# Optimization experiments

Hardware: AMD Instinct MI355X
Metric: run time of the kernel (lower is better)

## Reference

```python
import jax, jax.numpy as jnp
import numpy as np

NUM_EMBEDDINGS = 1024
EMBEDDING_DIM = 512
B, H, W = 32, 32, 32


def setup_inputs() -> dict:
    key = jax.random.key(0)
    k1, k2 = jax.random.split(key)
    z = jax.random.normal(k1, (B, EMBEDDING_DIM, H, W), dtype=jnp.float32)
    embedding = jax.random.normal(k2, (NUM_EMBEDDINGS, EMBEDDING_DIM), dtype=jnp.float32)
    return {"z": z, "embedding": embedding}


def reference(z, embedding):
    # z: [B, C, H, W] -> [B, H, W, C] -> [N, C]
    zp = jnp.transpose(z, (0, 2, 3, 1))
    b, h, w, d = zp.shape
    z_flat = zp.reshape(-1, d)
    # squared L2 distances: ||z||^2 - 2 z e^T + ||e||^2  -> [N, K]
    distances = (
        jnp.sum(z_flat ** 2, axis=1, keepdims=True)
        - 2.0 * (z_flat @ embedding.T)
        + jnp.sum(embedding ** 2, axis=1)
    )
    indices = jnp.argmin(distances, axis=1)  # [N]
    # one-hot @ embedding == direct gather
    quantized = embedding[indices]  # [N, d]
    quantized = quantized.reshape(b, h, w, d).transpose(0, 3, 1, 2)  # [B, C, H, W]
    return quantized, 0.0, indices.reshape(b, -1)
```

## Files before the change

### kernel.cpp

```cpp
#include <hip/hip_runtime.h>
#include <cfloat>

typedef _Float16 half8 __attribute__((ext_vector_type(8)));
typedef float    f32x4 __attribute__((ext_vector_type(4)));
typedef unsigned int  uint;
typedef unsigned short ushort;

constexpr int DIM  = 512;
constexpr int NEMB = 1024;
constexpr int HW   = 1024;
constexpr int NROW = 32 * HW;

constexpr long long QCOUNT = (long long)32 * 512 * 32 * 32;
constexpr long long SOFF   = QCOUNT;
constexpr long long IOFF   = SOFF + 1;

constexpr size_t WS_ZT    = 0;
constexpr size_t WS_ET    = 33554432;
constexpr size_t WS_ENORM = 34603008;
constexpr size_t WS_CNT   = 34607104;
constexpr size_t WS_LIST  = 34607360;
constexpr size_t WS_CANDB = WS_LIST + (size_t)NROW * 4;
constexpr size_t WS_CANDI = WS_CANDB + (size_t)2 * NROW * 8;
constexpr size_t WS_NEED  = WS_CANDI + (size_t)2 * NROW * 4;

constexpr float DELTA = 0.25f;

__device__ __forceinline__ void gld16(const void* g, void* l) {
    __builtin_amdgcn_global_load_lds(
        (const __attribute__((address_space(1))) void*)g,
        (__attribute__((address_space(3))) void*)l, 16, 0, 0);
}
union PKH8 { half8 v; _Float16 h[8]; };

__device__ __forceinline__ int swz_slot(int r, int g) {
    return g ^ ((r >> 1) & 3);
}

__global__ __launch_bounds__(256) void eprep(const float* __restrict__ e,
                                             char* __restrict__ et,
                                             float* __restrict__ enorm,
                                             int* __restrict__ cnt) {
    if (blockIdx.x == 0 && threadIdx.x == 0) *cnt = 0;
    int gid = blockIdx.x * 256 + threadIdx.x;
    int ke  = gid >> 6;
    int kbg = gid & 63;
    const float* src = e + (size_t)ke * DIM + kbg * 8;
    PKH8 h;
    float s = 0.f;
    #pragma unroll
    for (int j = 0; j < 8; ++j) {
        float v = src[j];
        h.h[j] = (_Float16)v;
        s += v * v;
    }
    int nc = ke >> 7, r = ke & 127, kc = kbg >> 2, g = kbg & 3;
    size_t byte = ((size_t)(nc * 16 + kc)) * 8192 + (size_t)r * 64
                + ((size_t)swz_slot(r, g) << 4);
    *reinterpret_cast<half8*>(et + byte) = h.v;
    #pragma unroll
    for (int off = 32; off > 0; off >>= 1) s += __shfl_down(s, off, 64);
    if (kbg == 0) enorm[ke] = s;
}

__global__ __launch_bounds__(256) void zprep(const float* __restrict__ z,
                                             char* __restrict__ zt) {
    __shared__ float ls[64][129];
    const int bx  = blockIdx.x;
    const int mb  = bx >> 3, kcc = bx & 7;
    const int b   = mb >> 3;
    const int hw0 = (mb & 7) * 128;
    const int t = threadIdx.x;
    for (int i = t; i < 64 * 128; i += 256) {
        int c = i >> 7, hw = i & 127;
        ls[c][hw] = z[((size_t)(b * DIM + kcc * 64 + c)) * HW + hw0 + hw];
    }
    __syncthreads();
    for (int j = t; j < 1024; j += 256) {
        int r = j >> 3, kbl = j & 7;
        PKH8 h;
        #pragma unroll
        for (int jj = 0; jj < 8; ++jj) h.h[jj] = (_Float16)ls[kbl * 8 + jj][r];
        int kc = kcc * 2 + (kbl >> 2), g = kbl & 3;
        size_t byte = ((size_t)(mb * 16 + kc)) * 8192 + (size_t)r * 64
                    + ((size_t)swz_slot(r, g) << 4);
        *reinterpret_cast<half8*>(zt + byte) = h.v;
    }
}

#define VQ_STAGE(SS, BUF)                                                      \
  {                                                                            \
    const int kc_ = (SS) & 15;                                                 \
    const size_t tB_ = ((size_t)((half4 + ((SS) >> 4)) * 16 + kc_)) * 8192;    \
    char* dst_ = smem + (BUF) * 16384;                                         \
    gld16(zt + zbase + (size_t)kc_ * 8192 + toff, dst_ + toff);                \
    gld16(et + tB_ + toff, dst_ + 8192 + toff);                                \
  }

#define VQ_STEP(S, VMLIT, BUF)                                                 \
  {                                                                            \
    asm volatile("s_waitcnt vmcnt(" VMLIT ")" ::: "memory");                   \
    __builtin_amdgcn_s_barrier();                                              \
    const char* buf_ = smem + (BUF) * 16384;                                   \
    half8 ah0 = *reinterpret_cast<const half8*>(buf_ + aoff0);                 \
    half8 ah1 = *reinterpret_cast<const half8*>(buf_ + aoff1);                 \
    half8 bh0 = *reinterpret_cast<const half8*>(buf_ + 8192 + boff0);          \
    half8 bh1 = *reinterpret_cast<const half8*>(buf_ + 8192 + boff1);          \
    half8 bh2 = *reinterpret_cast<const half8*>(buf_ + 8192 + boff2);          \
    half8 bh3 = *reinterpret_cast<const half8*>(buf_ + 8192 + boff3);          \
    asm volatile("s_waitcnt lgkmcnt(0)" ::: "memory");                         \
    __builtin_amdgcn_sched_barrier(0);                                         \
    __builtin_amdgcn_s_barrier();                                              \
    if ((S) + 4 < 64) VQ_STAGE((S) + 4, BUF);                                  \
    acc[0][0] = __builtin_amdgcn_mfma_f32_16x16x32_f16(ah0, bh0, acc[0][0], 0, 0, 0); \
    acc[0][1] = __builtin_amdgcn_mfma_f32_16x16x32_f16(ah0, bh1, acc[0][1], 0, 0, 0); \
    acc[0][2] = __builtin_amdgcn_mfma_f32_16x16x32_f16(ah0, bh2, acc[0][2], 0, 0, 0); \
    acc[0][3] = __builtin_amdgcn_mfma_f32_16x16x32_f16(ah0, bh3, acc[0][3], 0, 0, 0); \
    acc[1][0] = __builtin_amdgcn_mfma_f32_16x16x32_f16(ah1, bh0, acc[1][0], 0, 0, 0); \
    acc[1][1] = __builtin_amdgcn_mfma_f32_16x16x32_f16(ah1, bh1, acc[1][1], 0, 0, 0); \
    acc[1][2] = __builtin_amdgcn_mfma_f32_16x16x32_f16(ah1, bh2, acc[1][2], 0, 0, 0); \
    acc[1][3] = __builtin_amdgcn_mfma_f32_16x16x32_f16(ah1, bh3, acc[1][3], 0, 0, 0); \
    if (((S) & 15) == 15) {                                                    \
      const int ncl_ = ((S) >> 4) * 128;                                       \
      _Pragma("unroll")                                                        \
      for (int n = 0; n < 4; ++n) {                                            \
        const int lcol = ncl_ + wc * 64 + n * 16 + lr;                         \
        const float en = enorm_l[lcol];                                        \
        const int col = half * 512 + lcol;                                     \
        _Pragma("unroll")                                                      \
        for (int m = 0; m < 2; ++m) {                                          \
          _Pragma("unroll")                                                    \
          for (int q = 0; q < 4; ++q) {                                        \
            float dv = en - 2.0f * acc[m][n][q];                               \
            int sl = m * 4 + q;                                                \
            if (dv < b1v[sl]) { b2v[sl] = b1v[sl]; b1v[sl] = dv; i1v[sl] = col; } \
            else if (dv < b2v[sl]) b2v[sl] = dv;                               \
          }                                                                    \
        }                                                                      \
      }                                                                        \
      _Pragma("unroll")                                                        \
      for (int m = 0; m < 2; ++m)                                              \
        _Pragma("unroll")                                                      \
        for (int n = 0; n < 4; ++n) acc[m][n] = (f32x4)(0.f);                  \
    }                                                                          \
  }

__global__ __launch_bounds__(512, 4) void vq_mfma(const char* __restrict__ zt,
                                                  const char* __restrict__ et,
                                                  const float* __restrict__ enorm,
                                                  float2* __restrict__ cand_b,
                                                  int* __restrict__ cand_i) {
    __shared__ __align__(16) char smem[65536];
    __shared__ float enorm_l[512];

    const int t = threadIdx.x;
    const int w = t >> 6, l = t & 63;
    const int lr = l & 15, hg = l >> 4;
    const int wr = w >> 1;
    const int wc = w & 1;
    const int bid = blockIdx.x;
    const int mb = bid >> 1;
    const int half = bid & 1;
    const int half4 = half * 4;
    const int n0 = mb * 128;

    const int swz = swz_slot(lr, hg) << 4;
    const int aoff0 = (wr * 32 + lr) * 64 + swz;
    const int aoff1 = (wr * 32 + 16 + lr) * 64 + swz;
    const int boff0 = (wc * 64 + lr) * 64 + swz;
    const int boff1 = (wc * 64 + 16 + lr) * 64 + swz;
    const int boff2 = (wc * 64 + 32 + lr) * 64 + swz;
    const int boff3 = (wc * 64 + 48 + lr) * 64 + swz;

    enorm_l[t] = enorm[half * 512 + t];
    __syncthreads();

    float b1v[8], b2v[8]; int i1v[8];
    #pragma unroll
    for (int s = 0; s < 8; ++s) { b1v[s] = FLT_MAX; b2v[s] = FLT_MAX; i1v[s] = 0; }

    const size_t zbase = (size_t)mb * 16 * 8192;
    const int toff = t * 16;

    f32x4 acc[2][4];
    #pragma unroll
    for (int m = 0; m < 2; ++m)
        #pragma unroll
        for (int n = 0; n < 4; ++n) acc[m][n] = (f32x4)(0.f);

    VQ_STAGE(0, 0);
    VQ_STAGE(1, 1);
    VQ_STAGE(2, 2);
    VQ_STAGE(3, 3);

    for (int sp = 0; sp < 60; sp += 4) {
        VQ_STEP(sp + 0, "6", 0);
        VQ_STEP(sp + 1, "6", 1);
        VQ_STEP(sp + 2, "6", 2);
        VQ_STEP(sp + 3, "6", 3);
    }
    VQ_STEP(60, "6", 0);
    VQ_STEP(61, "4", 1);
    VQ_STEP(62, "2", 2);
    VQ_STEP(63, "0", 3);

    #pragma unroll
    for (int s = 0; s < 8; ++s) {
        #pragma unroll
        for (int off = 1; off <= 8; off <<= 1) {
            float ob1 = __shfl_xor(b1v[s], off, 64);
            int   oi1 = __shfl_xor(i1v[s], off, 64);
            float ob2 = __shfl_xor(b2v[s], off, 64);
            if (ob1 < b1v[s] || (ob1 == b1v[s] && oi1 < i1v[s])) {
                b2v[s] = fminf(b1v[s], ob2);
                b1v[s] = ob1; i1v[s] = oi1;
            } else {
                b2v[s] = fminf(b2v[s], ob1);
            }
        }
    }
    __syncthreads();
    float* red_b1 = reinterpret_cast<float*>(smem);
    float* red_b2 = reinterpret_cast<float*>(smem + 1024);
    int*   red_i1 = reinterpret_cast<int*>  (smem + 2048);
    if (lr == 0) {
        #pragma unroll
        for (int s = 0; s < 8; ++s) {
            int row = wr * 32 + (s >> 2) * 16 + hg * 4 + (s & 3);
            red_b1[row * 2 + wc] = b1v[s];
            red_b2[row * 2 + wc] = b2v[s];
            red_i1[row * 2 + wc] = i1v[s];
        }
    }
    __syncthreads();
    if (t < 128) {
        float a1 = red_b1[t * 2], a2 = red_b2[t * 2]; int ai = red_i1[t * 2];
        float c1 = red_b1[t * 2 + 1], c2 = red_b2[t * 2 + 1]; int ci = red_i1[t * 2 + 1];
        float B1, B2; int I1;
        if (c1 < a1 || (c1 == a1 && ci < ai)) { B1 = c1; I1 = ci; B2 = fminf(a1, c2); }
        else                                   { B1 = a1; I1 = ai; B2 = fminf(a2, c1); }
        cand_b[(size_t)half * NROW + n0 + t] = make_float2(B1, B2);
        cand_i[(size_t)half * NROW + n0 + t] = I1;
    }
}

__global__ __launch_bounds__(256) void combine(const float2* __restrict__ cand_b,
                                               const int* __restrict__ cand_i,
                                               const float* __restrict__ e,
                                               float* __restrict__ out,
                                               int* __restrict__ cnt,
                                               int* __restrict__ list) {
    __shared__ int idx_f[64];
    const int t = threadIdx.x;
    const int n0 = blockIdx.x * 64;
    if (t < 64) {
        const int row = n0 + t;
        float2 a = cand_b[row];
        float2 c = cand_b[NROW + row];
        int ai = cand_i[row];
        int ci = cand_i[NROW + row];
        float B1, B2; int I1;
        if (c.x < a.x) { B1 = c.x; I1 = ci; B2 = fminf(a.x, c.y); }
        else           { B1 = a.x; I1 = ai; B2 = fminf(a.y, c.x); }
        idx_f[t] = I1;
        out[IOFF + row] = (float)I1;
        if (B2 - B1 < DELTA) {
            int pos = atomicAdd(cnt, 1);
            list[pos] = row;
        }
    }
    if (blockIdx.x == 0 && t == 0) out[SOFF] = 0.0f;
    __syncthreads();

    const int b   = n0 >> 10;
    const int hw0 = n0 & (HW - 1);
    const int row4 = (t & 15) * 4;
    const int i0 = idx_f[row4 + 0];
    const int i1 = idx_f[row4 + 1];
    const int i2 = idx_f[row4 + 2];
    const int i3 = idx_f[row4 + 3];
    #pragma unroll 4
    for (int p = 0; p < 32; ++p) {
        int c = (t >> 4) + (p << 4);
        float4 v;
        v.x = e[(size_t)i0 * DIM + c];
        v.y = e[(size_t)i1 * DIM + c];
        v.z = e[(size_t)i2 * DIM + c];
        v.w = e[(size_t)i3 * DIM + c];
        *reinterpret_cast<float4*>(&out[((size_t)(b * DIM + c)) * HW + hw0 + row4]) = v;
    }
}

__global__ __launch_bounds__(256) void recheck(const float* __restrict__ z,
                                               const float* __restrict__ e,
                                               const float* __restrict__ enorm,
                                               const int* __restrict__ cnt,
                                               const int* __restrict__ list,
                                               float* __restrict__ out) {
    __shared__ float zrow[4][512];
    __shared__ float rb[256];
    __shared__ int   ri[256];
    __shared__ int   fidx[4];
    const int t = threadIdx.x;
    const int count = *cnt;
    const int ngrp = (count + 3) >> 2;
    for (int g = blockIdx.x; g < ngrp; g += gridDim.x) {
        const int base = g * 4;
        const int nr = min(4, count - base);
        __syncthreads();
        for (int r = 0; r < nr; ++r) {
            const int row = list[base + r];
            const int b = row >> 10, hw = row & (HW - 1);
            zrow[r][t]       = z[((size_t)(b * DIM + t))       * HW + hw];
            zrow[r][t + 256] = z[((size_t)(b * DIM + t + 256)) * HW + hw];
        }
        __syncthreads();
        float best[4]; int bi[4];
        #pragma unroll
        for (int r = 0; r < 4; ++r) { best[r] = FLT_MAX; bi[r] = 0; }
        #pragma unroll
        for (int p = 0; p < 4; ++p) {
            const int ke = t + p * 256;
            const float4* ep = reinterpret_cast<const float4*>(e + (size_t)ke * DIM);
            float d0 = 0.f, d1 = 0.f, d2 = 0.f, d3 = 0.f;
            const float4* z0 = reinterpret_cast<const float4*>(zrow[0]);
            const float4* z1 = reinterpret_cast<const float4*>(zrow[1]);
            const float4* z2 = reinterpret_cast<const float4*>(zrow[2]);
            const float4* z3 = reinterpret_cast<const float4*>(zrow[3]);
            for (int c = 0; c < 128; ++c) {
                float4 ev = ep[c];
                float4 a0 = z0[c], a1 = z1[c], a2 = z2[c], a3 = z3[c];
                d0 += ev.x*a0.x + ev.y*a0.y + ev.z*a0.z + ev.w*a0.w;
                d1 += ev.x*a1.x + ev.y*a1.y + ev.z*a1.z + ev.w*a1.w;
                d2 += ev.x*a2.x + ev.y*a2.y + ev.z*a2.z + ev.w*a2.w;
                d3 += ev.x*a3.x + ev.y*a3.y + ev.z*a3.z + ev.w*a3.w;
            }
            const float en = enorm[ke];
            float dd[4] = { en - 2.f*d0, en - 2.f*d1, en - 2.f*d2, en - 2.f*d3 };
            #pragma unroll
            for (int r = 0; r < 4; ++r)
                if (dd[r] < best[r]) { best[r] = dd[r]; bi[r] = ke; }
        }
        for (int r = 0; r < nr; ++r) {
            rb[t] = best[r]; ri[t] = bi[r];
            __syncthreads();
            #pragma unroll
            for (int s = 128; s > 0; s >>= 1) {
                if (t < s) {
                    float ov = rb[t + s]; int oi = ri[t + s];
                    if (ov < rb[t] || (ov == rb[t] && oi < ri[t])) {
                        rb[t] = ov; ri[t] = oi;
                    }
                }
                __syncthreads();
            }
            if (t == 0) {
                fidx[r] = ri[0];
                out[IOFF + list[base + r]] = (float)ri[0];
            }
            __syncthreads();
        }
        for (int r = 0; r < nr; ++r) {
            const int row = list[base + r];
            const int b = row >> 10, hw = row & (HW - 1);
            const int fbi = fidx[r];
            out[((size_t)(b * DIM + t))       * HW + hw] = e[(size_t)fbi * DIM + t];
            out[((size_t)(b * DIM + t + 256)) * HW + hw] = e[(size_t)fbi * DIM + t + 256];
        }
    }
}

constexpr int TM = 64;
constexpr int TN = 256;
constexpr int KC = 32;
constexpr int ZST = 68;
constexpr int EST = 260;

union F4 { float4 v; float f[4]; };

__global__ __launch_bounds__(256) void enorm_kernel(const float* __restrict__ e,
                                                    float* __restrict__ enorm) {
    int gid  = blockIdx.x * 256 + threadIdx.x;
    int wave = gid >> 6;
    int lane = gid & 63;
    if (wave >= NEMB) return;
    const float* row = e + (size_t)wave * DIM;
    float4 a = *reinterpret_cast<const float4*>(row + lane * 8);
    float4 b = *reinterpret_cast<const float4*>(row + lane * 8 + 4);
    float s = a.x*a.x + a.y*a.y + a.z*a.z + a.w*a.w
            + b.x*b.x + b.y*b.y + b.z*b.z + b.w*b.w;
    #pragma unroll
    for (int off = 32; off > 0; off >>= 1) s += __shfl_down(s, off, 64);
    if (lane == 0) enorm[wave] = s;
}

__global__ __launch_bounds__(256) void vq_main_kernel(const float* __restrict__ z,
                                                      const float* __restrict__ e,
                                                      const float* __restrict__ enorm,
                                                      float* __restrict__ out) {
    __shared__ float zs[KC][ZST];
    __shared__ float es[KC][EST];
    __shared__ float enorm_l[NEMB];
    __shared__ int   idx_f[TM];

    const int t   = threadIdx.x;
    const int n0  = blockIdx.x * TM;
    const int b   = n0 >> 10;
    const int hw0 = n0 & (HW - 1);
    const float* zb = z + ((size_t)b * DIM) * HW + hw0;

    #pragma unroll
    for (int i = 0; i < 4; ++i) enorm_l[t + i * 256] = enorm[t + i * 256];

    const int rg = t >> 5;
    const int cg = t & 31;

    float best[8];
    int   bidx[8];
    #pragma unroll
    for (int i = 0; i < 8; ++i) { best[i] = FLT_MAX; bidx[i] = 0; }

    const int z_r4 = (t & 15) * 4;
    const int z_c  = t >> 4;
    const int e_ke = t >> 3;
    const int e_c4 = t & 7;

    for (int nc = 0; nc < NEMB / TN; ++nc) {
        const int k0 = nc * TN;
        float acc[8][8];
        #pragma unroll
        for (int mi = 0; mi < 8; ++mi)
            #pragma unroll
            for (int nj = 0; nj < 8; ++nj) acc[mi][nj] = 0.f;

        for (int kc = 0; kc < DIM / KC; ++kc) {
            const int c0 = kc * KC;
            __syncthreads();
            #pragma unroll
            for (int p = 0; p < 2; ++p) {
                int c = z_c + p * 16;
                float4 v = *reinterpret_cast<const float4*>(zb + (size_t)(c0 + c) * HW + z_r4);
                *reinterpret_cast<float4*>(&zs[c][z_r4]) = v;
            }
            #pragma unroll
            for (int p = 0; p < 8; ++p) {
                int ke = e_ke + p * 32;
                float4 v = *reinterpret_cast<const float4*>(e + (size_t)(k0 + ke) * DIM + c0 + e_c4 * 4);
                es[e_c4 * 4 + 0][ke] = v.x;
                es[e_c4 * 4 + 1][ke] = v.y;
                es[e_c4 * 4 + 2][ke] = v.z;
                es[e_c4 * 4 + 3][ke] = v.w;
            }
            __syncthreads();
            #pragma unroll
            for (int kk = 0; kk < KC; ++kk) {
                F4 zf0, zf1, ef0, ef1;
                zf0.v = *reinterpret_cast<const float4*>(&zs[kk][rg * 8]);
                zf1.v = *reinterpret_cast<const float4*>(&zs[kk][rg * 8 + 4]);
                ef0.v = *reinterpret_cast<const float4*>(&es[kk][cg * 4]);
                ef1.v = *reinterpret_cast<const float4*>(&es[kk][128 + cg * 4]);
                #pragma unroll
                for (int mi = 0; mi < 4; ++mi) {
                    #pragma unroll
                    for (int nj = 0; nj < 4; ++nj) {
                        acc[mi][nj]         += zf0.f[mi] * ef0.f[nj];
                        acc[mi][nj + 4]     += zf0.f[mi] * ef1.f[nj];
                        acc[mi + 4][nj]     += zf1.f[mi] * ef0.f[nj];
                        acc[mi + 4][nj + 4] += zf1.f[mi] * ef1.f[nj];
                    }
                }
            }
        }
        #pragma unroll
        for (int mi = 0; mi < 8; ++mi) {
            #pragma unroll
            for (int nj = 0; nj < 8; ++nj) {
                int col = k0 + (nj < 4 ? cg * 4 + nj : 128 + cg * 4 + (nj - 4));
                float dv = enorm_l[col] - 2.0f * acc[mi][nj];
                if (dv < best[mi]) { best[mi] = dv; bidx[mi] = col; }
            }
        }
    }

    __syncthreads();
    float* best_l = reinterpret_cast<float*>(es);
    int*   idx_l  = reinterpret_cast<int*>(reinterpret_cast<char*>(es) + (size_t)TM * 33 * 4);
    #pragma unroll
    for (int mi = 0; mi < 8; ++mi) {
        int row = rg * 8 + mi;
        best_l[row * 33 + cg] = best[mi];
        idx_l[row * 33 + cg]  = bidx[mi];
    }
    __syncthreads();
    if (t < TM) {
        float bv = best_l[t * 33];
        int   bi = idx_l[t * 33];
        #pragma unroll
        for (int c = 1; c < 32; ++c) {
            float v  = best_l[t * 33 + c];
            int   ix = idx_l[t * 33 + c];
            if (v < bv || (v == bv && ix < bi)) { bv = v; bi = ix; }
        }
        idx_f[t] = bi;
        out[IOFF + n0 + t] = (float)bi;
    }
    if (blockIdx.x == 0 && t == 0) out[SOFF] = 0.0f;
    __syncthreads();

    const int row4 = (t & 15) * 4;
    const int i0 = idx_f[row4 + 0];
    const int i1 = idx_f[row4 + 1];
    const int i2 = idx_f[row4 + 2];
    const int i3 = idx_f[row4 + 3];
    #pragma unroll 4
    for (int p = 0; p < 32; ++p) {
        int c = (t >> 4) + (p << 4);
        float4 v;
        v.x = e[(size_t)i0 * DIM + c];
        v.y = e[(size_t)i1 * DIM + c];
        v.z = e[(size_t)i2 * DIM + c];
        v.w = e[(size_t)i3 * DIM + c];
        *reinterpret_cast<float4*>(&out[((size_t)(b * DIM + c)) * HW + hw0 + row4]) = v;
    }
}

extern "C" void kernel_launch(void* const* d_in, const int* in_sizes, int n_in,
                              void* d_out, int out_size, void* d_ws, size_t ws_size,
                              hipStream_t stream) {
    const float* z = (const float*)d_in[0];
    const float* e = (const float*)d_in[1];
    float* out = (float*)d_out;
    char*  ws  = (char*)d_ws;

    if (ws_size >= WS_NEED) {
        char*   zt     = ws + WS_ZT;
        char*   et     = ws + WS_ET;
        float*  enorm  = (float*)(ws + WS_ENORM);
        int*    cnt    = (int*)(ws + WS_CNT);
        int*    list   = (int*)(ws + WS_LIST);
        float2* cand_b = (float2*)(ws + WS_CANDB);
        int*    cand_i = (int*)(ws + WS_CANDI);

        hipLaunchKernelGGL(eprep,   dim3(256),            dim3(256), 0, stream, e, et, enorm, cnt);
        hipLaunchKernelGGL(zprep,   dim3(2048),           dim3(256), 0, stream, z, zt);
        hipLaunchKernelGGL(vq_mfma, dim3(NROW / 128 * 2), dim3(512), 0, stream,
                           zt, et, enorm, cand_b, cand_i);
        hipLaunchKernelGGL(combine, dim3(NROW / 64),      dim3(256), 0, stream,
                           cand_b, cand_i, e, out, cnt, list);
        hipLaunchKernelGGL(recheck, dim3(1024),           dim3(256), 0, stream,
                           z, e, enorm, cnt, list, out);
    } else {
        float* enorm = (float*)ws;
        hipLaunchKernelGGL(enorm_kernel,   dim3(NEMB / 4), dim3(256), 0, stream, e, enorm);
        hipLaunchKernelGGL(vq_main_kernel, dim3(NROW / TM), dim3(256), 0, stream,
                           z, e, enorm, out);
    }
}
```

Measured before the change: 219.8 us.

## Double K-tile depth to 64 with 8-slot swizzle and two-stage pipeline

Changes the fp16 staging layout of z and the codebook from 32-wide K chunks (64-byte rows, 4-slot XOR swizzle) to 64-wide chunks (128-byte rows, 8-slot swizzle). Each pipeline step now loads twice the data and issues 16 MFMAs instead of 8. The pipeline goes from 4 stages of 16KB to 2 stages of 32KB, which halves the number of barrier pairs per tile. In exchange the prefetch distance is shorter, so memory latency may be less well hidden.

```diff
diff --git a/kernel.cpp b/kernel.cpp
--- a/kernel.cpp
+++ b/kernel.cpp
@@ -33,8 +33,8 @@
 }
 union PKH8 { half8 v; _Float16 h[8]; };
 
-__device__ __forceinline__ int swz_slot(int r, int g) {
-    return g ^ ((r >> 1) & 3);
+__device__ __forceinline__ int swz8(int r, int g) {
+    return g ^ (r & 7);
 }
 
 __global__ __launch_bounds__(256) void eprep(const float* __restrict__ e,
@@ -54,9 +54,9 @@
         h.h[j] = (_Float16)v;
         s += v * v;
     }
-    int nc = ke >> 7, r = ke & 127, kc = kbg >> 2, g = kbg & 3;
-    size_t byte = ((size_t)(nc * 16 + kc)) * 8192 + (size_t)r * 64
-                + ((size_t)swz_slot(r, g) << 4);
+    int nc = ke >> 7, r = ke & 127, kc64 = kbg >> 3, g = kbg & 7;
+    size_t byte = ((size_t)(nc * 8 + kc64)) * 16384 + (size_t)r * 128
+                + ((size_t)swz8(r, g) << 4);
     *reinterpret_cast<half8*>(et + byte) = h.v;
     #pragma unroll
     for (int off = 32; off > 0; off >>= 1) s += __shfl_down(s, off, 64);
@@ -77,51 +77,66 @@
     }
     __syncthreads();
     for (int j = t; j < 1024; j += 256) {
-        int r = j >> 3, kbl = j & 7;
+        int r = j >> 3, g = j & 7;
         PKH8 h;
         #pragma unroll
-        for (int jj = 0; jj < 8; ++jj) h.h[jj] = (_Float16)ls[kbl * 8 + jj][r];
-        int kc = kcc * 2 + (kbl >> 2), g = kbl & 3;
-        size_t byte = ((size_t)(mb * 16 + kc)) * 8192 + (size_t)r * 64
-                    + ((size_t)swz_slot(r, g) << 4);
+        for (int jj = 0; jj < 8; ++jj) h.h[jj] = (_Float16)ls[g * 8 + jj][r];
+        size_t byte = ((size_t)(mb * 8 + kcc)) * 16384 + (size_t)r * 128
+                    + ((size_t)swz8(r, g) << 4);
         *reinterpret_cast<half8*>(zt + byte) = h.v;
     }
 }
 
 #define VQ_STAGE(SS, BUF)                                                      \
   {                                                                            \
-    const int kc_ = (SS) & 15;                                                 \
-    const size_t tB_ = ((size_t)((half4 + ((SS) >> 4)) * 16 + kc_)) * 8192;    \
-    char* dst_ = smem + (BUF) * 16384;                                         \
-    gld16(zt + zbase + (size_t)kc_ * 8192 + toff, dst_ + toff);                \
-    gld16(et + tB_ + toff, dst_ + 8192 + toff);                                \
+    const int kc_ = (SS) & 7;                                                  \
+    const size_t tB_ = ((size_t)((half4 + ((SS) >> 3)) * 8 + kc_)) * 16384;    \
+    char* dst_ = smem + (BUF) * 32768;                                         \
+    gld16(zt + zbase + (size_t)kc_ * 16384 + toff,        dst_ + toff);        \
+    gld16(zt + zbase + (size_t)kc_ * 16384 + 8192 + toff, dst_ + 8192 + toff); \
+    gld16(et + tB_ + toff,        dst_ + 16384 + toff);                        \
+    gld16(et + tB_ + 8192 + toff, dst_ + 24576 + toff);                        \
   }
 
 #define VQ_STEP(S, VMLIT, BUF)                                                 \
   {                                                                            \
     asm volatile("s_waitcnt vmcnt(" VMLIT ")" ::: "memory");                   \
     __builtin_amdgcn_s_barrier();                                              \
-    const char* buf_ = smem + (BUF) * 16384;                                   \
-    half8 ah0 = *reinterpret_cast<const half8*>(buf_ + aoff0);                 \
-    half8 ah1 = *reinterpret_cast<const half8*>(buf_ + aoff1);                 \
-    half8 bh0 = *reinterpret_cast<const half8*>(buf_ + 8192 + boff0);          \
-    half8 bh1 = *reinterpret_cast<const half8*>(buf_ + 8192 + boff1);          \
-    half8 bh2 = *reinterpret_cast<const half8*>(buf_ + 8192 + boff2);          \
-    half8 bh3 = *reinterpret_cast<const half8*>(buf_ + 8192 + boff3);          \
+    const char* buf_ = smem + (BUF) * 32768;                                   \
+    half8 a00 = *reinterpret_cast<const half8*>(buf_ + aoff0);                 \
+    half8 a01 = *reinterpret_cast<const half8*>(buf_ + aoff1);                 \
+    half8 a10 = *reinterpret_cast<const half8*>(buf_ + (aoff0 ^ 64));          \
+    half8 a11 = *reinterpret_cast<const half8*>(buf_ + (aoff1 ^ 64));          \
+    half8 b00 = *reinterpret_cast<const half8*>(buf_ + 16384 + boff0);         \
+    half8 b01 = *reinterpret_cast<const half8*>(buf_ + 16384 + boff1);         \
+    half8 b02 = *reinterpret_cast<const half8*>(buf_ + 16384 + boff2);         \
+    half8 b03 = *reinterpret_cast<const half8*>(buf_ + 16384 + boff3);         \
+    half8 b10 = *reinterpret_cast<const half8*>(buf_ + 16384 + (boff0 ^ 64));  \
+    half8 b11 = *reinterpret_cast<const half8*>(buf_ + 16384 + (boff1 ^ 64));  \
+    half8 b12 = *reinterpret_cast<const half8*>(buf_ + 16384 + (boff2 ^ 64));  \
+    half8 b13 = *reinterpret_cast<const half8*>(buf_ + 16384 + (boff3 ^ 64));  \
     asm volatile("s_waitcnt lgkmcnt(0)" ::: "memory");                         \
     __builtin_amdgcn_sched_barrier(0);                                         \
     __builtin_amdgcn_s_barrier();                                              \
-    if ((S) + 4 < 64) VQ_STAGE((S) + 4, BUF);                                  \
-    acc[0][0] = __builtin_amdgcn_mfma_f32_16x16x32_f16(ah0, bh0, acc[0][0], 0, 0, 0); \
-    acc[0][1] = __builtin_amdgcn_mfma_f32_16x16x32_f16(ah0, bh1, acc[0][1], 0, 0, 0); \
-    acc[0][2] = __builtin_amdgcn_mfma_f32_16x16x32_f16(ah0, bh2, acc[0][2], 0, 0, 0); \
-    acc[0][3] = __builtin_amdgcn_mfma_f32_16x16x32_f16(ah0, bh3, acc[0][3], 0, 0, 0); \
-    acc[1][0] = __builtin_amdgcn_mfma_f32_16x16x32_f16(ah1, bh0, acc[1][0], 0, 0, 0); \
-    acc[1][1] = __builtin_amdgcn_mfma_f32_16x16x32_f16(ah1, bh1, acc[1][1], 0, 0, 0); \
-    acc[1][2] = __builtin_amdgcn_mfma_f32_16x16x32_f16(ah1, bh2, acc[1][2], 0, 0, 0); \
-    acc[1][3] = __builtin_amdgcn_mfma_f32_16x16x32_f16(ah1, bh3, acc[1][3], 0, 0, 0); \
-    if (((S) & 15) == 15) {                                                    \
-      const int ncl_ = ((S) >> 4) * 128;                                       \
+    if ((S) + 2 < 32) VQ_STAGE((S) + 2, BUF);                                  \
+    acc[0][0] = __builtin_amdgcn_mfma_f32_16x16x32_f16(a00, b00, acc[0][0], 0, 0, 0); \
+    acc[0][1] = __builtin_amdgcn_mfma_f32_16x16x32_f16(a00, b01, acc[0][1], 0, 0, 0); \
+    acc[0][2] = __builtin_amdgcn_mfma_f32_16x16x32_f16(a00, b02, acc[0][2], 0, 0, 0); \
+    acc[0][3] = __builtin_amdgcn_mfma_f32_16x16x32_f16(a00, b03, acc[0][3], 0, 0, 0); \
+    acc[1][0] = __builtin_amdgcn_mfma_f32_16x16x32_f16(a01, b00, acc[1][0], 0, 0, 0); \
+    acc[1][1] = __builtin_amdgcn_mfma_f32_16x16x32_f16(a01, b01, acc[1][1], 0, 0, 0); \
+    acc[1][2] = __builtin_amdgcn_mfma_f32_16x16x32_f16(a01, b02, acc[1][2], 0, 0, 0); \
+    acc[1][3] = __builtin_amdgcn_mfma_f32_16x16x32_f16(a01, b03, acc[1][3], 0, 0, 0); \
+    acc[0][0] = __builtin_amdgcn_mfma_f32_16x16x32_f16(a10, b10, acc[0][0], 0, 0, 0); \
+    acc[0][1] = __builtin_amdgcn_mfma_f32_16x16x32_f16(a10, b11, acc[0][1], 0, 0, 0); \
+    acc[0][2] = __builtin_amdgcn_mfma_f32_16x16x32_f16(a10, b12, acc[0][2], 0, 0, 0); \
+    acc[0][3] = __builtin_amdgcn_mfma_f32_16x16x32_f16(a10, b13, acc[0][3], 0, 0, 0); \
+    acc[1][0] = __builtin_amdgcn_mfma_f32_16x16x32_f16(a11, b10, acc[1][0], 0, 0, 0); \
+    acc[1][1] = __builtin_amdgcn_mfma_f32_16x16x32_f16(a11, b11, acc[1][1], 0, 0, 0); \
+    acc[1][2] = __builtin_amdgcn_mfma_f32_16x16x32_f16(a11, b12, acc[1][2], 0, 0, 0); \
+    acc[1][3] = __builtin_amdgcn_mfma_f32_16x16x32_f16(a11, b13, acc[1][3], 0, 0, 0); \
+    if (((S) & 7) == 7) {                                                      \
+      const int ncl_ = ((S) >> 3) * 128;                                       \
       _Pragma("unroll")                                                        \
       for (int n = 0; n < 4; ++n) {                                            \
         const int lcol = ncl_ + wc * 64 + n * 16 + lr;                         \
@@ -164,13 +179,13 @@
     const int half4 = half * 4;
     const int n0 = mb * 128;
 
-    const int swz = swz_slot(lr, hg) << 4;
-    const int aoff0 = (wr * 32 + lr) * 64 + swz;
-    const int aoff1 = (wr * 32 + 16 + lr) * 64 + swz;
-    const int boff0 = (wc * 64 + lr) * 64 + swz;
-    const int boff1 = (wc * 64 + 16 + lr) * 64 + swz;
-    const int boff2 = (wc * 64 + 32 + lr) * 64 + swz;
-    const int boff3 = (wc * 64 + 48 + lr) * 64 + swz;
+    const int swz = swz8(lr, hg) << 4;
+    const int aoff0 = (wr * 32 + lr) * 128 + swz;
+    const int aoff1 = (wr * 32 + 16 + lr) * 128 + swz;
+    const int boff0 = (wc * 64 + lr) * 128 + swz;
+    const int boff1 = (wc * 64 + 16 + lr) * 128 + swz;
+    const int boff2 = (wc * 64 + 32 + lr) * 128 + swz;
+    const int boff3 = (wc * 64 + 48 + lr) * 128 + swz;
 
     enorm_l[t] = enorm[half * 512 + t];
     __syncthreads();
@@ -179,7 +194,7 @@
     #pragma unroll
     for (int s = 0; s < 8; ++s) { b1v[s] = FLT_MAX; b2v[s] = FLT_MAX; i1v[s] = 0; }
 
-    const size_t zbase = (size_t)mb * 16 * 8192;
+    const size_t zbase = (size_t)mb * 8 * 16384;
     const int toff = t * 16;
 
     f32x4 acc[2][4];
@@ -190,19 +205,13 @@
 
     VQ_STAGE(0, 0);
     VQ_STAGE(1, 1);
-    VQ_STAGE(2, 2);
-    VQ_STAGE(3, 3);
-
-    for (int sp = 0; sp < 60; sp += 4) {
-        VQ_STEP(sp + 0, "6", 0);
-        VQ_STEP(sp + 1, "6", 1);
-        VQ_STEP(sp + 2, "6", 2);
-        VQ_STEP(sp + 3, "6", 3);
-    }
-    VQ_STEP(60, "6", 0);
-    VQ_STEP(61, "4", 1);
-    VQ_STEP(62, "2", 2);
-    VQ_STEP(63, "0", 3);
+
+    for (int sp = 0; sp < 30; sp += 2) {
+        VQ_STEP(sp + 0, "4", 0);
+        VQ_STEP(sp + 1, "4", 1);
+    }
+    VQ_STEP(30, "4", 0);
+    VQ_STEP(31, "0", 1);
 
     #pragma unroll
     for (int s = 0; s < 8; ++s) {
```

Measured after the change: 218.3 us. About the same (-0.7%).

## Split codebook into quarters per block, shrink LDS pipeline, merge prep kernels

Applied to the files above, without the earlier changes.

The distance kernel now splits the 1024-entry codebook into four quarters of 256 instead of two halves, launching twice as many blocks. The LDS staging ring drops from four buffers to two (32 KB), and launch bounds request 8 waves per SIMD for higher occupancy. The combine step merges four candidate partials instead of two, and the two prep kernels are fused into one launch to save a kernel launch. In exchange, the z tile is reloaded by four blocks instead of two, and the shallower pipeline exposes more global load latency per block.

```diff
diff --git a/kernel.cpp b/kernel.cpp
--- a/kernel.cpp
+++ b/kernel.cpp
@@ -21,8 +21,8 @@
 constexpr size_t WS_CNT   = 34607104;
 constexpr size_t WS_LIST  = 34607360;
 constexpr size_t WS_CANDB = WS_LIST + (size_t)NROW * 4;
-constexpr size_t WS_CANDI = WS_CANDB + (size_t)2 * NROW * 8;
-constexpr size_t WS_NEED  = WS_CANDI + (size_t)2 * NROW * 4;
+constexpr size_t WS_CANDI = WS_CANDB + (size_t)4 * NROW * 8;
+constexpr size_t WS_NEED  = WS_CANDI + (size_t)4 * NROW * 4;
 
 constexpr float DELTA = 0.25f;
 
@@ -33,44 +33,46 @@
 }
 union PKH8 { half8 v; _Float16 h[8]; };
 
-__device__ __forceinline__ int swz_slot(int r, int g) {
+__device__ __forceinline__ int swz4(int r, int g) {
     return g ^ ((r >> 1) & 3);
 }
 
-__global__ __launch_bounds__(256) void eprep(const float* __restrict__ e,
-                                             char* __restrict__ et,
-                                             float* __restrict__ enorm,
-                                             int* __restrict__ cnt) {
-    if (blockIdx.x == 0 && threadIdx.x == 0) *cnt = 0;
-    int gid = blockIdx.x * 256 + threadIdx.x;
-    int ke  = gid >> 6;
-    int kbg = gid & 63;
-    const float* src = e + (size_t)ke * DIM + kbg * 8;
-    PKH8 h;
-    float s = 0.f;
-    #pragma unroll
-    for (int j = 0; j < 8; ++j) {
-        float v = src[j];
-        h.h[j] = (_Float16)v;
-        s += v * v;
-    }
-    int nc = ke >> 7, r = ke & 127, kc = kbg >> 2, g = kbg & 3;
-    size_t byte = ((size_t)(nc * 16 + kc)) * 8192 + (size_t)r * 64
-                + ((size_t)swz_slot(r, g) << 4);
-    *reinterpret_cast<half8*>(et + byte) = h.v;
-    #pragma unroll
-    for (int off = 32; off > 0; off >>= 1) s += __shfl_down(s, off, 64);
-    if (kbg == 0) enorm[ke] = s;
-}
-
-__global__ __launch_bounds__(256) void zprep(const float* __restrict__ z,
-                                             char* __restrict__ zt) {
+__global__ __launch_bounds__(256) void prep(const float* __restrict__ z,
+                                            const float* __restrict__ e,
+                                            char* __restrict__ zt,
+                                            char* __restrict__ et,
+                                            float* __restrict__ enorm,
+                                            int* __restrict__ cnt) {
     __shared__ float ls[64][129];
-    const int bx  = blockIdx.x;
+    const int bx = blockIdx.x;
+    const int t  = threadIdx.x;
+    if (bx >= 2048) {
+        const int eb = bx - 2048;
+        if (eb == 0 && t == 0) *cnt = 0;
+        int gid = eb * 256 + t;
+        int ke  = gid >> 6;
+        int kbg = gid & 63;
+        const float* src = e + (size_t)ke * DIM + kbg * 8;
+        PKH8 h;
+        float s = 0.f;
+        #pragma unroll
+        for (int j = 0; j < 8; ++j) {
+            float v = src[j];
+            h.h[j] = (_Float16)v;
+            s += v * v;
+        }
+        int nc = ke >> 7, r = ke & 127, kc = kbg >> 2, g = kbg & 3;
+        size_t byte = ((size_t)(nc * 16 + kc)) * 8192 + (size_t)r * 64
+                    + ((size_t)swz4(r, g) << 4);
+        *reinterpret_cast<half8*>(et + byte) = h.v;
+        #pragma unroll
+        for (int off = 32; off > 0; off >>= 1) s += __shfl_down(s, off, 64);
+        if (kbg == 0) enorm[ke] = s;
+        return;
+    }
     const int mb  = bx >> 3, kcc = bx & 7;
     const int b   = mb >> 3;
     const int hw0 = (mb & 7) * 128;
-    const int t = threadIdx.x;
     for (int i = t; i < 64 * 128; i += 256) {
         int c = i >> 7, hw = i & 127;
         ls[c][hw] = z[((size_t)(b * DIM + kcc * 64 + c)) * HW + hw0 + hw];
@@ -83,15 +85,16 @@
         for (int jj = 0; jj < 8; ++jj) h.h[jj] = (_Float16)ls[kbl * 8 + jj][r];
         int kc = kcc * 2 + (kbl >> 2), g = kbl & 3;
         size_t byte = ((size_t)(mb * 16 + kc)) * 8192 + (size_t)r * 64
-                    + ((size_t)swz_slot(r, g) << 4);
+                    + ((size_t)swz4(r, g) << 4);
         *reinterpret_cast<half8*>(zt + byte) = h.v;
     }
 }
 
 #define VQ_STAGE(SS, BUF)                                                      \
   {                                                                            \
-    const int kc_ = (SS) & 15;                                                 \
-    const size_t tB_ = ((size_t)((half4 + ((SS) >> 4)) * 16 + kc_)) * 8192;    \
+    const int kc_  = (SS) & 15;                                                \
+    const int ncl_ = (SS) >> 4;                                                \
+    const size_t tB_ = ((size_t)((q2 + ncl_) * 16 + kc_)) * 8192;              \
     char* dst_ = smem + (BUF) * 16384;                                         \
     gld16(zt + zbase + (size_t)kc_ * 8192 + toff, dst_ + toff);                \
     gld16(et + tB_ + toff, dst_ + 8192 + toff);                                \
@@ -102,37 +105,37 @@
     asm volatile("s_waitcnt vmcnt(" VMLIT ")" ::: "memory");                   \
     __builtin_amdgcn_s_barrier();                                              \
     const char* buf_ = smem + (BUF) * 16384;                                   \
-    half8 ah0 = *reinterpret_cast<const half8*>(buf_ + aoff0);                 \
-    half8 ah1 = *reinterpret_cast<const half8*>(buf_ + aoff1);                 \
-    half8 bh0 = *reinterpret_cast<const half8*>(buf_ + 8192 + boff0);          \
-    half8 bh1 = *reinterpret_cast<const half8*>(buf_ + 8192 + boff1);          \
-    half8 bh2 = *reinterpret_cast<const half8*>(buf_ + 8192 + boff2);          \
-    half8 bh3 = *reinterpret_cast<const half8*>(buf_ + 8192 + boff3);          \
+    half8 a00 = *reinterpret_cast<const half8*>(buf_ + aoff0);                 \
+    half8 a01 = *reinterpret_cast<const half8*>(buf_ + aoff1);                 \
+    half8 b00 = *reinterpret_cast<const half8*>(buf_ + 8192 + boff0);          \
+    half8 b01 = *reinterpret_cast<const half8*>(buf_ + 8192 + boff1);          \
+    half8 b02 = *reinterpret_cast<const half8*>(buf_ + 8192 + boff2);          \
+    half8 b03 = *reinterpret_cast<const half8*>(buf_ + 8192 + boff3);          \
     asm volatile("s_waitcnt lgkmcnt(0)" ::: "memory");                         \
     __builtin_amdgcn_sched_barrier(0);                                         \
     __builtin_amdgcn_s_barrier();                                              \
-    if ((S) + 4 < 64) VQ_STAGE((S) + 4, BUF);                                  \
-    acc[0][0] = __builtin_amdgcn_mfma_f32_16x16x32_f16(ah0, bh0, acc[0][0], 0, 0, 0); \
-    acc[0][1] = __builtin_amdgcn_mfma_f32_16x16x32_f16(ah0, bh1, acc[0][1], 0, 0, 0); \
-    acc[0][2] = __builtin_amdgcn_mfma_f32_16x16x32_f16(ah0, bh2, acc[0][2], 0, 0, 0); \
-    acc[0][3] = __builtin_amdgcn_mfma_f32_16x16x32_f16(ah0, bh3, acc[0][3], 0, 0, 0); \
-    acc[1][0] = __builtin_amdgcn_mfma_f32_16x16x32_f16(ah1, bh0, acc[1][0], 0, 0, 0); \
-    acc[1][1] = __builtin_amdgcn_mfma_f32_16x16x32_f16(ah1, bh1, acc[1][1], 0, 0, 0); \
-    acc[1][2] = __builtin_amdgcn_mfma_f32_16x16x32_f16(ah1, bh2, acc[1][2], 0, 0, 0); \
-    acc[1][3] = __builtin_amdgcn_mfma_f32_16x16x32_f16(ah1, bh3, acc[1][3], 0, 0, 0); \
+    if ((S) + 2 < 32) VQ_STAGE((S) + 2, BUF);                                  \
+    acc[0][0] = __builtin_amdgcn_mfma_f32_16x16x32_f16(a00, b00, acc[0][0], 0, 0, 0); \
+    acc[0][1] = __builtin_amdgcn_mfma_f32_16x16x32_f16(a00, b01, acc[0][1], 0, 0, 0); \
+    acc[0][2] = __builtin_amdgcn_mfma_f32_16x16x32_f16(a00, b02, acc[0][2], 0, 0, 0); \
+    acc[0][3] = __builtin_amdgcn_mfma_f32_16x16x32_f16(a00, b03, acc[0][3], 0, 0, 0); \
+    acc[1][0] = __builtin_amdgcn_mfma_f32_16x16x32_f16(a01, b00, acc[1][0], 0, 0, 0); \
+    acc[1][1] = __builtin_amdgcn_mfma_f32_16x16x32_f16(a01, b01, acc[1][1], 0, 0, 0); \
+    acc[1][2] = __builtin_amdgcn_mfma_f32_16x16x32_f16(a01, b02, acc[1][2], 0, 0, 0); \
+    acc[1][3] = __builtin_amdgcn_mfma_f32_16x16x32_f16(a01, b03, acc[1][3], 0, 0, 0); \
     if (((S) & 15) == 15) {                                                    \
-      const int ncl_ = ((S) >> 4) * 128;                                       \
+      const int ncl_ = (S) >> 4;                                               \
       _Pragma("unroll")                                                        \
       for (int n = 0; n < 4; ++n) {                                            \
-        const int lcol = ncl_ + wc * 64 + n * 16 + lr;                         \
+        const int lcol = ncl_ * 128 + wc * 64 + n * 16 + lr;                   \
         const float en = enorm_l[lcol];                                        \
-        const int col = half * 512 + lcol;                                     \
+        const int col = q * 256 + lcol;                                        \
         _Pragma("unroll")                                                      \
         for (int m = 0; m < 2; ++m) {                                          \
           _Pragma("unroll")                                                    \
-          for (int q = 0; q < 4; ++q) {                                        \
-            float dv = en - 2.0f * acc[m][n][q];                               \
-            int sl = m * 4 + q;                                                \
+          for (int qq = 0; qq < 4; ++qq) {                                     \
+            float dv = en - 2.0f * acc[m][n][qq];                              \
+            int sl = m * 4 + qq;                                               \
             if (dv < b1v[sl]) { b2v[sl] = b1v[sl]; b1v[sl] = dv; i1v[sl] = col; } \
             else if (dv < b2v[sl]) b2v[sl] = dv;                               \
           }                                                                    \
@@ -145,13 +148,13 @@
     }                                                                          \
   }
 
-__global__ __launch_bounds__(512, 4) void vq_mfma(const char* __restrict__ zt,
+__global__ __launch_bounds__(512, 8) void vq_mfma(const char* __restrict__ zt,
                                                   const char* __restrict__ et,
                                                   const float* __restrict__ enorm,
                                                   float2* __restrict__ cand_b,
                                                   int* __restrict__ cand_i) {
-    __shared__ __align__(16) char smem[65536];
-    __shared__ float enorm_l[512];
+    __shared__ __align__(16) char smem[32768];
+    __shared__ float enorm_l[256];
 
     const int t = threadIdx.x;
     const int w = t >> 6, l = t & 63;
@@ -159,12 +162,12 @@
     const int wr = w >> 1;
     const int wc = w & 1;
     const int bid = blockIdx.x;
-    const int mb = bid >> 1;
-    const int half = bid & 1;
-    const int half4 = half * 4;
+    const int mb = bid >> 2;
+    const int q  = bid & 3;
+    const int q2 = q * 2;
     const int n0 = mb * 128;
 
-    const int swz = swz_slot(lr, hg) << 4;
+    const int swz = swz4(lr, hg) << 4;
     const int aoff0 = (wr * 32 + lr) * 64 + swz;
     const int aoff1 = (wr * 32 + 16 + lr) * 64 + swz;
     const int boff0 = (wc * 64 + lr) * 64 + swz;
@@ -172,7 +175,7 @@
     const int boff2 = (wc * 64 + 32 + lr) * 64 + swz;
     const int boff3 = (wc * 64 + 48 + lr) * 64 + swz;
 
-    enorm_l[t] = enorm[half * 512 + t];
+    if (t < 256) enorm_l[t] = enorm[q * 256 + t];
     __syncthreads();
 
     float b1v[8], b2v[8]; int i1v[8];
@@ -190,19 +193,13 @@
 
     VQ_STAGE(0, 0);
     VQ_STAGE(1, 1);
-    VQ_STAGE(2, 2);
-    VQ_STAGE(3, 3);
-
-    for (int sp = 0; sp < 60; sp += 4) {
-        VQ_STEP(sp + 0, "6", 0);
-        VQ_STEP(sp + 1, "6", 1);
-        VQ_STEP(sp + 2, "6", 2);
-        VQ_STEP(sp + 3, "6", 3);
-    }
-    VQ_STEP(60, "6", 0);
-    VQ_STEP(61, "4", 1);
-    VQ_STEP(62, "2", 2);
-    VQ_STEP(63, "0", 3);
+
+    for (int sp = 0; sp < 30; sp += 2) {
+        VQ_STEP(sp + 0, "2", 0);
+        VQ_STEP(sp + 1, "2", 1);
+    }
+    VQ_STEP(30, "2", 0);
+    VQ_STEP(31, "0", 1);
 
     #pragma unroll
     for (int s = 0; s < 8; ++s) {
@@ -239,8 +236,8 @@
         float B1, B2; int I1;
         if (c1 < a1 || (c1 == a1 && ci < ai)) { B1 = c1; I1 = ci; B2 = fminf(a1, c2); }
         else                                   { B1 = a1; I1 = ai; B2 = fminf(a2, c1); }
-        cand_b[(size_t)half * NROW + n0 + t] = make_float2(B1, B2);
-        cand_i[(size_t)half * NROW + n0 + t] = I1;
+        cand_b[(size_t)q * NROW + n0 + t] = make_float2(B1, B2);
+        cand_i[(size_t)q * NROW + n0 + t] = I1;
     }
 }
 
@@ -256,12 +253,15 @@
     if (t < 64) {
         const int row = n0 + t;
         float2 a = cand_b[row];
-        float2 c = cand_b[NROW + row];
-        int ai = cand_i[row];
-        int ci = cand_i[NROW + row];
-        float B1, B2; int I1;
-        if (c.x < a.x) { B1 = c.x; I1 = ci; B2 = fminf(a.x, c.y); }
-        else           { B1 = a.x; I1 = ai; B2 = fminf(a.y, c.x); }
+        float B1 = a.x, B2 = a.y;
+        int   I1 = cand_i[row];
+        #pragma unroll
+        for (int qq = 1; qq < 4; ++qq) {
+            float2 c = cand_b[(size_t)qq * NROW + row];
+            int    ci = cand_i[(size_t)qq * NROW + row];
+            if (c.x < B1) { B2 = fminf(B1, c.y); B1 = c.x; I1 = ci; }
+            else          { B2 = fminf(B2, c.x); }
+        }
         idx_f[t] = I1;
         out[IOFF + row] = (float)I1;
         if (B2 - B1 < DELTA) {
@@ -541,9 +541,9 @@
         float2* cand_b = (float2*)(ws + WS_CANDB);
         int*    cand_i = (int*)(ws + WS_CANDI);
 
-        hipLaunchKernelGGL(eprep,   dim3(256),            dim3(256), 0, stream, e, et, enorm, cnt);
-        hipLaunchKernelGGL(zprep,   dim3(2048),           dim3(256), 0, stream, z, zt);
-        hipLaunchKernelGGL(vq_mfma, dim3(NROW / 128 * 2), dim3(512), 0, stream,
+        hipLaunchKernelGGL(prep,    dim3(2304),           dim3(256), 0, stream,
+                           z, e, zt, et, enorm, cnt);
+        hipLaunchKernelGGL(vq_mfma, dim3(NROW / 128 * 4), dim3(512), 0, stream,
                            zt, et, enorm, cand_b, cand_i);
         hipLaunchKernelGGL(combine, dim3(NROW / 64),      dim3(256), 0, stream,
                            cand_b, cand_i, e, out, cnt, list);
```

Result: slower. 261.6 us (+19.0%).
